# Kernel tuning notes

Hardware: AMD Instinct MI355X
Metric: run time of the kernel (lower is better)

The kernel has to match this reference:

```python
import jax, jax.numpy as jnp
import numpy as np

B, N, ESM_DIM, D, K = 256, 100000, 1280, 512, 8
ATT_TAU = 1.0
NEG_INF_FILL = -10000.0
EPS = 1e-6


def _l2norm(x, axis=-1):
    return x / jnp.linalg.norm(x, axis=axis, keepdims=True).clip(1e-12)


def setup_inputs() -> dict:
    key = jax.random.key(0)
    ks = jax.random.split(key, 8)
    index_emb = _l2norm(jax.random.normal(ks[0], (N, ESM_DIM), jnp.float32))
    return {
        "query_esm_pooled": jax.random.normal(ks[1], (B, ESM_DIM), jnp.float32),
        "model_embs": jax.random.normal(ks[2], (B, D), jnp.float32),
        "index_emb": index_emb,
        "index_labels": jax.random.randint(ks[3], (N,), 0, 2, jnp.int64),
        "exclude_idx": jax.random.randint(ks[4], (B,), 0, N, jnp.int64),
        "proj_W": jax.random.normal(ks[5], (ESM_DIM, D), jnp.float32) * 0.02,
        "proj_b": jnp.zeros((D,), jnp.float32),
        "clf_W": jax.random.normal(ks[6], (2 * D, 2), jnp.float32) * 0.02,
        "clf_b": jnp.zeros((2,), jnp.float32),
    }


def reference(query_esm_pooled, model_embs, index_emb, index_labels, exclude_idx,
              proj_W, proj_b, clf_W, clf_b):
    # esm_dim != model_emb_dim -> use ESM-pooled queries, project neighbors
    Q = _l2norm(query_esm_pooled)                       # [B, E]
    sims = Q @ index_emb.T                              # [B, N] cosine (index pre-normalized)
    sims = sims.at[jnp.arange(B), exclude_idx].set(NEG_INF_FILL)
    _, topk = jax.lax.top_k(sims, K)                    # [B, K]

    neigh_raw = index_emb[topk]                         # [B, K, E]
    neigh_lbl = index_labels[topk]                      # [B, K]
    neigh_proj = neigh_raw @ proj_W + proj_b            # [B, K, D]

    # tiny cross-attention: query = model_embs, keys/values = neighbors
    scale = 1.0 / (jnp.sqrt(jnp.float32(D)) * ATT_TAU)
    att = jax.nn.softmax(jnp.einsum('bd,bkd->bk', model_embs, neigh_proj) * scale, axis=-1)
    z_neigh = jnp.einsum('bk,bkd->bd', att, neigh_proj)  # [B, D]

    logits_retr = jnp.concatenate([model_embs, z_neigh], axis=1) @ clf_W + clf_b  # [B, 2]

    # prototypes (detached, matching torch.no_grad)
    mask_pos = (neigh_lbl == 1).astype(jnp.float32)     # [B, K]
    mask_neg = (neigh_lbl == 0).astype(jnp.float32)
    pos_proto = jnp.einsum('bk,bkd->bd', mask_pos, neigh_proj) / (mask_pos.sum(1, keepdims=True) + EPS)
    neg_proto = jnp.einsum('bk,bkd->bd', mask_neg, neigh_proj) / (mask_neg.sum(1, keepdims=True) + EPS)
    pos_proto = jax.lax.stop_gradient(pos_proto)
    neg_proto = jax.lax.stop_gradient(neg_proto)

    retr_align_loss = jnp.mean((model_embs - pos_proto) ** 2) - 0.5 * jnp.mean((model_embs - neg_proto) ** 2)
    return logits_retr, retr_align_loss
```

## Files before the change

### kernel.cpp

```cpp
#include <hip/hip_runtime.h>
#include <math.h>

#define B_SZ 256
#define N_SZ 100000
#define E_SZ 1280
#define D_SZ 512

#define NCH 1563

typedef __attribute__((ext_vector_type(8))) short s8v;
typedef __attribute__((ext_vector_type(4))) float f32x4;

__device__ __forceinline__ unsigned short f2bf(float f) {
  unsigned int u = __float_as_uint(f);
  u += 0x7fffu + ((u >> 16) & 1u);
  return (unsigned short)(u >> 16);
}
__device__ __forceinline__ unsigned int pack2(float a, float b) {
  return (unsigned)f2bf(a) | ((unsigned)f2bf(b) << 16);
}

__device__ __forceinline__ void gload16(const void* g, void* l) {
  __builtin_amdgcn_global_load_lds(
      (const __attribute__((address_space(1))) void*)g,
      (__attribute__((address_space(3))) void*)l, 16, 0, 0);
}

#define TOP8_UPDATE(v_, i_)                                                 \
  if ((v_) > minv) {                                                        \
    _Pragma("unroll")                                                       \
    for (int s_ = 0; s_ < 8; ++s_)                                          \
      if (s_ == mins) { bv[s_] = (v_); bi[s_] = (i_); }                     \
    minv = bv[0]; mins = 0;                                                 \
    _Pragma("unroll")                                                       \
    for (int s_ = 1; s_ < 8; ++s_)                                          \
      if (bv[s_] < minv) { minv = bv[s_]; mins = s_; }                      \
  }

__global__ __launch_bounds__(256) void k_normq(const float* __restrict__ q,
                                               unsigned short* __restrict__ qn) {
  __shared__ float red[4];
  int row = blockIdx.x, t = threadIdx.x;
  const float* src = q + (size_t)row * E_SZ;
  float x[5];
  float ss = 0.f;
#pragma unroll
  for (int i = 0; i < 5; ++i) { x[i] = src[t + 256 * i]; ss += x[i] * x[i]; }
#pragma unroll
  for (int o = 32; o > 0; o >>= 1) ss += __shfl_down(ss, o, 64);
  if ((t & 63) == 0) red[t >> 6] = ss;
  __syncthreads();
  float nrm = sqrtf(red[0] + red[1] + red[2] + red[3]);
  nrm = fmaxf(nrm, 1e-12f);
  float inv = 1.0f / nrm;
  unsigned short* dst = qn + (size_t)row * E_SZ;
#pragma unroll
  for (int i = 0; i < 5; ++i) dst[t + 256 * i] = f2bf(x[i] * inv);
}

__global__ __launch_bounds__(256) void k_wt(const float* __restrict__ W,
                                            unsigned short* __restrict__ Wt) {
  __shared__ float T[64][65];
  const int kb = blockIdx.x * 64;
  const int nb = blockIdx.y * 64;
  const int t = threadIdx.x;
#pragma unroll
  for (int i = 0; i < 16; ++i) {
    int kr = i * 4 + (t >> 6);
    T[kr][t & 63] = W[(size_t)(kb + kr) * D_SZ + nb + (t & 63)];
  }
  __syncthreads();
  const int n = t >> 2, ks = (t & 3) * 16;
  unsigned int ow[8];
#pragma unroll
  for (int j = 0; j < 8; ++j)
    ow[j] = (unsigned)f2bf(T[ks + 2 * j][n]) |
            ((unsigned)f2bf(T[ks + 2 * j + 1][n]) << 16);
  unsigned short* dst = Wt + (size_t)(nb + n) * E_SZ + kb + ks;
  *(uint4*)dst = make_uint4(ow[0], ow[1], ow[2], ow[3]);
  *(uint4*)(dst + 8) = make_uint4(ow[4], ow[5], ow[6], ow[7]);
}

__global__ __launch_bounds__(256) void k_sims_topk(
    const unsigned short* __restrict__ qn, const float* __restrict__ emb,
    const int* __restrict__ excl, float* __restrict__ cval) {
  __shared__ __align__(16) char lds[40960];
  const int t = threadIdx.x;
  const int l = t & 63, w = t >> 6;
  const int r15 = l & 15, g = l >> 4;
  const int jbase = blockIdx.x * 64;
  const int myq = (w << 6) + l;
  const int ex = excl[myq];

  f32x4 acc[4][4];
#pragma unroll
  for (int i = 0; i < 4; ++i)
#pragma unroll
    for (int j = 0; j < 4; ++j) acc[i][j] = (f32x4)0.f;

  const int chunk = (t & 3) ^ ((t >> 3) & 3);
  const unsigned short* aSrc0 = qn + (size_t)(t >> 2) * E_SZ + chunk * 8;
  const int grow = min(jbase + (t >> 2), N_SZ - 1);
  const float* bSrc = emb + (size_t)grow * E_SZ + chunk * 8;
  const int bwr = t * 16;

  const int fsw = ((g ^ ((r15 >> 1) & 3)) << 4);
  int afoff[4], bfoff[4];
#pragma unroll
  for (int mq = 0; mq < 4; ++mq)
    afoff[mq] = ((w << 6) + mq * 16 + r15) * 64 + fsw;
#pragma unroll
  for (int nj = 0; nj < 4; ++nj)
    bfoff[nj] = (nj * 16 + r15) * 64 + fsw;

  float4 bw0[2], bw1[2];

#define STAGEA(kt_, aoff_)                                                   \
  { _Pragma("unroll") for (int i_ = 0; i_ < 4; ++i_)                         \
      gload16(aSrc0 + (size_t)i_ * (64 * E_SZ) + (kt_),                      \
              lds + (aoff_) + i_ * 4096 + w * 1024); }
#define LOADB(br_, kt_)                                                      \
  { br_[0] = *(const float4*)(bSrc + (kt_));                                 \
    br_[1] = *(const float4*)(bSrc + (kt_) + 4); }
#define CVTWR(br_, boff_)                                                    \
  { uint4 p_;                                                                \
    p_.x = pack2(br_[0].x, br_[0].y); p_.y = pack2(br_[0].z, br_[0].w);      \
    p_.z = pack2(br_[1].x, br_[1].y); p_.w = pack2(br_[1].z, br_[1].w);      \
    *(uint4*)(lds + (boff_) + bwr) = p_; }
#define COMPUTE(aoff_, boff_)                                                \
  { s8v af_[4];                                                              \
    _Pragma("unroll") for (int mq_ = 0; mq_ < 4; ++mq_)                      \
      af_[mq_] = *(const s8v*)(lds + (aoff_) + afoff[mq_]);                  \
    _Pragma("unroll") for (int nj_ = 0; nj_ < 4; ++nj_) {                    \
      s8v bf_ = *(const s8v*)(lds + (boff_) + bfoff[nj_]);                   \
      _Pragma("unroll") for (int mq_ = 0; mq_ < 4; ++mq_)                    \
        acc[mq_][nj_] = __builtin_amdgcn_mfma_f32_16x16x32_bf16(             \
            af_[mq_], bf_, acc[mq_][nj_], 0, 0, 0);                          \
    } }
#define FENCE2                                                               \
  { asm volatile("s_waitcnt vmcnt(2) lgkmcnt(0)" ::: "memory");              \
    __builtin_amdgcn_s_barrier(); }
#define FENCE0                                                               \
  { asm volatile("s_waitcnt vmcnt(0) lgkmcnt(0)" ::: "memory");              \
    __builtin_amdgcn_s_barrier(); }

  STAGEA(0, 0);
  LOADB(bw0, 0);
  LOADB(bw1, 32);
  CVTWR(bw0, 32768);
  FENCE2;

  for (int s = 0; s < 40; s += 2) {
    STAGEA((s + 1) * 32, 16384);
    if (s + 2 < 40) LOADB(bw0, (s + 2) * 32);
    COMPUTE(0, 32768);
    CVTWR(bw1, 36864);
    if (s + 2 < 40) { FENCE2; } else { FENCE0; }
    if (s + 2 < 40) STAGEA((s + 2) * 32, 0);
    if (s + 3 < 40) LOADB(bw1, (s + 3) * 32);
    COMPUTE(16384, 36864);
    if (s + 2 < 40) CVTWR(bw0, 32768);
    if (s + 3 < 40) { FENCE2; } else { FENCE0; }
  }

  for (int ph = 0; ph < 2; ++ph) {
    if ((w >> 1) == ph) {
      float* Sbuf = (float*)(lds + (w & 1) * 16640);
#pragma unroll
      for (int mq = 0; mq < 4; ++mq)
#pragma unroll
        for (int nj = 0; nj < 4; ++nj)
#pragma unroll
          for (int r = 0; r < 4; ++r)
            Sbuf[(16 * mq + 4 * g + r) * 65 + 16 * nj + r15] = acc[mq][nj][r];
      float bv[8]; int bi[8];
#pragma unroll
      for (int s = 0; s < 8; ++s) { bv[s] = -1e30f; bi[s] = 0; }
      float minv = -1e30f; int mins = 0;
      const float* Srow = Sbuf + l * 65;
      for (int c = 0; c < 64; ++c) {
        int gj = jbase + c;
        float v = Srow[c];
        if (gj < N_SZ && gj != ex) { TOP8_UPDATE(v, gj); }
      }
      float* vdst = cval + (size_t)blockIdx.x * 4096 + myq * 8;
      *(float4*)vdst = make_float4(bv[0], bv[1], bv[2], bv[3]);
      *(float4*)(vdst + 4) = make_float4(bv[4], bv[5], bv[6], bv[7]);
      int* idst = (int*)(cval + (size_t)blockIdx.x * 4096 + 2048) + myq * 8;
      *(int4*)idst = make_int4(bi[0], bi[1], bi[2], bi[3]);
      *(int4*)(idst + 4) = make_int4(bi[4], bi[5], bi[6], bi[7]);
    }
    __syncthreads();
  }
#undef STAGEA
#undef LOADB
#undef CVTWR
#undef COMPUTE
#undef FENCE2
#undef FENCE0
}

__global__ __launch_bounds__(256) void k_merge(const float* __restrict__ cval,
                                               int* __restrict__ topk) {
  __shared__ float sv[2048];
  __shared__ int si[2048];
  const int q = blockIdx.x, t = threadIdx.x;
  float bv[8]; int bi[8];
#pragma unroll
  for (int s = 0; s < 8; ++s) { bv[s] = -1e30f; bi[s] = 0; }
  float minv = -1e30f; int mins = 0;
  for (int c = t; c < NCH; c += 256) {
    const float* vp = cval + (size_t)c * 4096 + q * 8;
    const int* ip = (const int*)(cval + (size_t)c * 4096 + 2048) + q * 8;
    float4 v0 = *(const float4*)vp, v1 = *(const float4*)(vp + 4);
    int4 i0 = *(const int4*)ip, i1 = *(const int4*)(ip + 4);
    float va[8] = {v0.x, v0.y, v0.z, v0.w, v1.x, v1.y, v1.z, v1.w};
    int ia[8] = {i0.x, i0.y, i0.z, i0.w, i1.x, i1.y, i1.z, i1.w};
#pragma unroll
    for (int s = 0; s < 8; ++s) {
      float v = va[s]; int ix = ia[s];
      TOP8_UPDATE(v, ix);
    }
  }
#pragma unroll
  for (int s = 0; s < 8; ++s) { sv[t * 8 + s] = bv[s]; si[t * 8 + s] = bi[s]; }
  __syncthreads();
  if (t < 64) {
    for (int rr = 1; rr < 4; ++rr) {
      int r = t + rr * 64;
#pragma unroll
      for (int s = 0; s < 8; ++s) {
        float v = sv[r * 8 + s]; int ix = si[r * 8 + s];
        TOP8_UPDATE(v, ix);
      }
    }
#pragma unroll
    for (int s = 0; s < 8; ++s) { sv[t * 8 + s] = bv[s]; si[t * 8 + s] = bi[s]; }
  }
  __syncthreads();
  if (t < 8) {
    for (int rr = 1; rr < 8; ++rr) {
      int r = t + rr * 8;
#pragma unroll
      for (int s = 0; s < 8; ++s) {
        float v = sv[r * 8 + s]; int ix = si[r * 8 + s];
        TOP8_UPDATE(v, ix);
      }
    }
#pragma unroll
    for (int s = 0; s < 8; ++s) { sv[t * 8 + s] = bv[s]; si[t * 8 + s] = bi[s]; }
  }
  __syncthreads();
  if (t == 0) {
    for (int r = 1; r < 8; ++r) {
#pragma unroll
      for (int s = 0; s < 8; ++s) {
        float v = sv[r * 8 + s]; int ix = si[r * 8 + s];
        TOP8_UPDATE(v, ix);
      }
    }
#pragma unroll
    for (int s = 0; s < 8; ++s) topk[q * 8 + s] = bi[s];
  }
}

__global__ __launch_bounds__(256) void k_proj(
    const float* __restrict__ emb, const int* __restrict__ topk,
    const unsigned short* __restrict__ Wt, const float* __restrict__ bias,
    float* __restrict__ nproj) {
  __shared__ __align__(16) char lds[65536];
  const int t = threadIdx.x, l = t & 63, w = t >> 6;
  const int r15 = l & 15, g = l >> 4;
  const int wm = w >> 1, wn = w & 1;
  const int r0 = blockIdx.x * 128, n0 = blockIdx.y * 128;
  const int sr = t >> 3, kc = t & 7;

  int grow[4];
#pragma unroll
  for (int i = 0; i < 4; ++i) grow[i] = topk[r0 + i * 32 + sr];

  int woff[4];
#pragma unroll
  for (int i = 0; i < 4; ++i) {
    int row = i * 32 + sr;
    woff[i] = row * 128 + (((kc + (row & 7)) & 7) << 4);
  }
  int afoff[2][4], bfoff[2][4];
#pragma unroll
  for (int h = 0; h < 2; ++h) {
#pragma unroll
    for (int qq = 0; qq < 4; ++qq) {
      int rowa = 64 * wm + 16 * qq + r15;
      afoff[h][qq] = rowa * 128 + ((((h << 2) + g + (rowa & 7)) & 7) << 4);
      int rowb = 64 * wn + 16 * qq + r15;
      bfoff[h][qq] = rowb * 128 + ((((h << 2) + g + (rowb & 7)) & 7) << 4);
    }
  }

  f32x4 acc[4][4];
#pragma unroll
  for (int i = 0; i < 4; ++i)
#pragma unroll
    for (int j = 0; j < 4; ++j) acc[i][j] = (f32x4)0.f;

  float4 aset[4][2];
  s8v bset[4];

#define PLOADA(kt_)                                                          \
  { _Pragma("unroll") for (int i_ = 0; i_ < 4; ++i_) {                       \
      const float* s_ = emb + (size_t)grow[i_] * E_SZ + (kt_) + kc * 8;      \
      aset[i_][0] = *(const float4*)s_;                                      \
      aset[i_][1] = *(const float4*)(s_ + 4); } }
#define PLOADB(kt_)                                                          \
  { _Pragma("unroll") for (int i_ = 0; i_ < 4; ++i_)                         \
      bset[i_] = *(const s8v*)(Wt + (size_t)(n0 + i_ * 32 + sr) * E_SZ +     \
                               (kt_) + kc * 8); }
#define PWR(bA_, bB_)                                                        \
  { _Pragma("unroll") for (int i_ = 0; i_ < 4; ++i_) {                       \
      uint4 p_;                                                              \
      p_.x = pack2(aset[i_][0].x, aset[i_][0].y);                            \
      p_.y = pack2(aset[i_][0].z, aset[i_][0].w);                            \
      p_.z = pack2(aset[i_][1].x, aset[i_][1].y);                            \
      p_.w = pack2(aset[i_][1].z, aset[i_][1].w);                            \
      *(uint4*)((bA_) + woff[i_]) = p_;                                      \
      *(s8v*)((bB_) + woff[i_]) = bset[i_]; } }
#define PCOMP(bA_, bB_)                                                      \
  { _Pragma("unroll") for (int h_ = 0; h_ < 2; ++h_) {                       \
      s8v af_[4], bf_[4];                                                    \
      _Pragma("unroll") for (int q_ = 0; q_ < 4; ++q_) {                     \
        af_[q_] = *(const s8v*)((bA_) + afoff[h_][q_]);                      \
        bf_[q_] = *(const s8v*)((bB_) + bfoff[h_][q_]); }                    \
      _Pragma("unroll") for (int nj_ = 0; nj_ < 4; ++nj_)                    \
        _Pragma("unroll") for (int mq_ = 0; mq_ < 4; ++mq_)                  \
          acc[mq_][nj_] = __builtin_amdgcn_mfma_f32_16x16x32_bf16(           \
              af_[mq_], bf_[nj_], acc[mq_][nj_], 0, 0, 0); } }

  PLOADA(0); PLOADB(0);
  PWR(lds, lds + 32768);
  __syncthreads();
  for (int s = 0; s < 20; ++s) {
    char* cA = lds + (s & 1) * 16384;
    char* cB = lds + 32768 + (s & 1) * 16384;
    char* nA = lds + ((s + 1) & 1) * 16384;
    char* nB = lds + 32768 + ((s + 1) & 1) * 16384;
    if (s + 1 < 20) { PLOADA((s + 1) * 64); PLOADB((s + 1) * 64); }
    PCOMP(cA, cB);
    if (s + 1 < 20) { PWR(nA, nB); }
    __syncthreads();
  }
#pragma unroll
  for (int nj = 0; nj < 4; ++nj) {
    int n = n0 + 64 * wn + 16 * nj + r15;
    float bn = bias[n];
#pragma unroll
    for (int mq = 0; mq < 4; ++mq) {
      int m = r0 + 64 * wm + 16 * mq + 4 * g;
#pragma unroll
      for (int r = 0; r < 4; ++r)
        nproj[(size_t)(m + r) * D_SZ + n] = acc[mq][nj][r] + bn;
    }
  }
#undef PLOADA
#undef PLOADB
#undef PWR
#undef PCOMP
}

__global__ __launch_bounds__(256) void k_attn(
    const float* __restrict__ model, const float* __restrict__ proj,
    const int* __restrict__ topk, const int* __restrict__ labels,
    const float* __restrict__ clfW, const float* __restrict__ clfb,
    float* __restrict__ out, float* __restrict__ lossp) {
  __shared__ float P[8 * 512];
  __shared__ float red[4];
  int b = blockIdx.x, t = threadIdx.x;
  const float* src = proj + (size_t)b * 8 * 512;
#pragma unroll
  for (int i = 0; i < 4; ++i) {
    int o = i * 1024 + t * 4;
    *(float4*)&P[o] = *(const float4*)&src[o];
  }
  __syncthreads();
  float m0 = model[b * 512 + t], m1 = model[b * 512 + 256 + t];

  float sc[8];
#pragma unroll
  for (int k = 0; k < 8; ++k) {
    float p = m0 * P[k * 512 + t] + m1 * P[k * 512 + 256 + t];
#pragma unroll
    for (int o = 32; o > 0; o >>= 1) p += __shfl_down(p, o, 64);
    if ((t & 63) == 0) red[t >> 6] = p;
    __syncthreads();
    sc[k] = red[0] + red[1] + red[2] + red[3];
    __syncthreads();
  }
  const float scale = 0.04419417382415922f;
  float mx = -1e30f;
  float s_[8];
#pragma unroll
  for (int k = 0; k < 8; ++k) { s_[k] = sc[k] * scale; mx = fmaxf(mx, s_[k]); }
  float den = 0.f, att[8];
#pragma unroll
  for (int k = 0; k < 8; ++k) { att[k] = expf(s_[k] - mx); den += att[k]; }
  float iden = 1.0f / den;
#pragma unroll
  for (int k = 0; k < 8; ++k) att[k] *= iden;

  float z0 = 0.f, z1 = 0.f;
#pragma unroll
  for (int k = 0; k < 8; ++k) {
    z0 = fmaf(att[k], P[k * 512 + t], z0);
    z1 = fmaf(att[k], P[k * 512 + 256 + t], z1);
  }
#pragma unroll
  for (int c = 0; c < 2; ++c) {
    float lp = m0 * clfW[t * 2 + c] + m1 * clfW[(t + 256) * 2 + c] +
               z0 * clfW[(512 + t) * 2 + c] + z1 * clfW[(768 + t) * 2 + c];
#pragma unroll
    for (int o = 32; o > 0; o >>= 1) lp += __shfl_down(lp, o, 64);
    if ((t & 63) == 0) red[t >> 6] = lp;
    __syncthreads();
    if (t == 0) out[b * 2 + c] = red[0] + red[1] + red[2] + red[3] + clfb[c];
    __syncthreads();
  }
  float cp = 0.f, cn = 0.f;
  float p0 = 0.f, p1 = 0.f, n0 = 0.f, n1 = 0.f;
#pragma unroll
  for (int k = 0; k < 8; ++k) {
    int lb = labels[topk[b * 8 + k]];
    float mp = (lb == 1) ? 1.f : 0.f;
    float mn = (lb == 0) ? 1.f : 0.f;
    cp += mp; cn += mn;
    p0 = fmaf(mp, P[k * 512 + t], p0);
    p1 = fmaf(mp, P[k * 512 + 256 + t], p1);
    n0 = fmaf(mn, P[k * 512 + t], n0);
    n1 = fmaf(mn, P[k * 512 + 256 + t], n1);
  }
  float icp = 1.0f / (cp + 1e-6f), icn = 1.0f / (cn + 1e-6f);
  p0 *= icp; p1 *= icp; n0 *= icn; n1 *= icn;
  float lq = (m0 - p0) * (m0 - p0) + (m1 - p1) * (m1 - p1) -
             0.5f * ((m0 - n0) * (m0 - n0) + (m1 - n1) * (m1 - n1));
#pragma unroll
  for (int o = 32; o > 0; o >>= 1) lq += __shfl_down(lq, o, 64);
  if ((t & 63) == 0) red[t >> 6] = lq;
  __syncthreads();
  if (t == 0) lossp[b] = red[0] + red[1] + red[2] + red[3];
}

__global__ __launch_bounds__(256) void k_loss(const float* __restrict__ lossp,
                                              float* __restrict__ out) {
  __shared__ float red[4];
  int t = threadIdx.x;
  float v = lossp[t];
#pragma unroll
  for (int o = 32; o > 0; o >>= 1) v += __shfl_down(v, o, 64);
  if ((t & 63) == 0) red[t >> 6] = v;
  __syncthreads();
  if (t == 0)
    out[512] = (red[0] + red[1] + red[2] + red[3]) * (1.0f / (256.0f * 512.0f));
}

extern "C" void kernel_launch(void* const* d_in, const int* in_sizes, int n_in,
                              void* d_out, int out_size, void* d_ws,
                              size_t ws_size, hipStream_t stream) {
  (void)in_sizes; (void)n_in; (void)out_size; (void)ws_size;
  const float* q      = (const float*)d_in[0];
  const float* model  = (const float*)d_in[1];
  const float* emb    = (const float*)d_in[2];
  const int*   labels = (const int*)d_in[3];
  const int*   excl   = (const int*)d_in[4];
  const float* projW  = (const float*)d_in[5];
  const float* projb  = (const float*)d_in[6];
  const float* clfW   = (const float*)d_in[7];
  const float* clfb   = (const float*)d_in[8];
  float* out = (float*)d_out;

  char* ws = (char*)d_ws;
  unsigned short* qn = (unsigned short*)ws;
  unsigned short* Wt = (unsigned short*)(ws + 655360);
  float* cval  = (float*)(ws + 1966080);
  int*   topk  = (int*)(ws + 27574272);
  float* nproj = (float*)(ws + 27582464);
  float* lossp = (float*)(ws + 31776768);

  k_normq<<<256, 256, 0, stream>>>(q, qn);
  k_wt<<<dim3(20, 8), 256, 0, stream>>>(projW, Wt);
  k_sims_topk<<<NCH, 256, 0, stream>>>(qn, emb, excl, cval);
  k_merge<<<256, 256, 0, stream>>>(cval, topk);
  k_proj<<<dim3(16, 4), 256, 0, stream>>>(emb, topk, Wt, projb, nproj);
  k_attn<<<256, 256, 0, stream>>>(model, nproj, topk, labels, clfW, clfb, out, lossp);
  k_loss<<<1, 256, 0, stream>>>(lossp, out);
}
```

Before: 412.1 us.

## Load MFMA operands directly from global into registers, bypassing LDS staging

Replaces the LDS-staged, barrier-synchronised double-buffered GEMM in the similarity/top-k kernel with direct global-to-register loads of the A and B fragments, register double-buffering and no per-step barriers. The fp32-to-bf16 packing now uses the HIP bf16 intrinsic. The epilogue scan switches to a 68-float padded row read as float4. This removes LDS traffic and barrier stalls, but every wave now fetches its own copy of the shared B tile and the query rows. That multiplies global and L2 traffic and raises register pressure.

```diff
diff --git a/kernel.cpp b/kernel.cpp
--- a/kernel.cpp
+++ b/kernel.cpp
@@ -1,4 +1,5 @@
 #include <hip/hip_runtime.h>
+#include <hip/hip_bf16.h>
 #include <math.h>
 
 #define B_SZ 256
@@ -17,13 +18,9 @@
   return (unsigned short)(u >> 16);
 }
 __device__ __forceinline__ unsigned int pack2(float a, float b) {
-  return (unsigned)f2bf(a) | ((unsigned)f2bf(b) << 16);
-}
-
-__device__ __forceinline__ void gload16(const void* g, void* l) {
-  __builtin_amdgcn_global_load_lds(
-      (const __attribute__((address_space(1))) void*)g,
-      (__attribute__((address_space(3))) void*)l, 16, 0, 0);
+  union { __hip_bfloat162 h; unsigned u; } c;
+  c.h = __float22bfloat162_rn(make_float2(a, b));
+  return c.u;
 }
 
 #define TOP8_UPDATE(v_, i_)                                                 \
@@ -84,7 +81,7 @@
 __global__ __launch_bounds__(256) void k_sims_topk(
     const unsigned short* __restrict__ qn, const float* __restrict__ emb,
     const int* __restrict__ excl, float* __restrict__ cval) {
-  __shared__ __align__(16) char lds[40960];
+  __shared__ __align__(16) float Sbuf[2][64 * 68];
   const int t = threadIdx.x;
   const int l = t & 63, w = t >> 6;
   const int r15 = l & 15, g = l >> 4;
@@ -98,90 +95,89 @@
 #pragma unroll
     for (int j = 0; j < 4; ++j) acc[i][j] = (f32x4)0.f;
 
-  const int chunk = (t & 3) ^ ((t >> 3) & 3);
-  const unsigned short* aSrc0 = qn + (size_t)(t >> 2) * E_SZ + chunk * 8;
-  const int grow = min(jbase + (t >> 2), N_SZ - 1);
-  const float* bSrc = emb + (size_t)grow * E_SZ + chunk * 8;
-  const int bwr = t * 16;
-
-  const int fsw = ((g ^ ((r15 >> 1) & 3)) << 4);
-  int afoff[4], bfoff[4];
+  const unsigned short* aP[4];
 #pragma unroll
   for (int mq = 0; mq < 4; ++mq)
-    afoff[mq] = ((w << 6) + mq * 16 + r15) * 64 + fsw;
-#pragma unroll
-  for (int nj = 0; nj < 4; ++nj)
-    bfoff[nj] = (nj * 16 + r15) * 64 + fsw;
-
-  float4 bw0[2], bw1[2];
-
-#define STAGEA(kt_, aoff_)                                                   \
+    aP[mq] = qn + (size_t)((w << 6) + 16 * mq + r15) * E_SZ + g * 8;
+  const float* bP[4];
+#pragma unroll
+  for (int nj = 0; nj < 4; ++nj) {
+    int jr = min(jbase + 16 * nj + r15, N_SZ - 1);
+    bP[nj] = emb + (size_t)jr * E_SZ + g * 8;
+  }
+
+  s8v aA[4], aB[4];
+  float4 braw[4][2];
+
+#define LOADA(dst_, kt_)                                                     \
   { _Pragma("unroll") for (int i_ = 0; i_ < 4; ++i_)                         \
-      gload16(aSrc0 + (size_t)i_ * (64 * E_SZ) + (kt_),                      \
-              lds + (aoff_) + i_ * 4096 + w * 1024); }
-#define LOADB(br_, kt_)                                                      \
-  { br_[0] = *(const float4*)(bSrc + (kt_));                                 \
-    br_[1] = *(const float4*)(bSrc + (kt_) + 4); }
-#define CVTWR(br_, boff_)                                                    \
-  { uint4 p_;                                                                \
-    p_.x = pack2(br_[0].x, br_[0].y); p_.y = pack2(br_[0].z, br_[0].w);      \
-    p_.z = pack2(br_[1].x, br_[1].y); p_.w = pack2(br_[1].z, br_[1].w);      \
-    *(uint4*)(lds + (boff_) + bwr) = p_; }
-#define COMPUTE(aoff_, boff_)                                                \
-  { s8v af_[4];                                                              \
-    _Pragma("unroll") for (int mq_ = 0; mq_ < 4; ++mq_)                      \
-      af_[mq_] = *(const s8v*)(lds + (aoff_) + afoff[mq_]);                  \
-    _Pragma("unroll") for (int nj_ = 0; nj_ < 4; ++nj_) {                    \
-      s8v bf_ = *(const s8v*)(lds + (boff_) + bfoff[nj_]);                   \
+      dst_[i_] = *(const s8v*)(aP[i_] + (kt_)); }
+#define LOADB(kt_)                                                           \
+  { _Pragma("unroll") for (int i_ = 0; i_ < 4; ++i_) {                       \
+      braw[i_][0] = *(const float4*)(bP[i_] + (kt_));                        \
+      braw[i_][1] = *(const float4*)(bP[i_] + (kt_) + 4); } }
+#define PACKB(bb_)                                                           \
+  { _Pragma("unroll") for (int i_ = 0; i_ < 4; ++i_) {                       \
+      union { uint4 u; s8v s; } c_;                                          \
+      c_.u.x = pack2(braw[i_][0].x, braw[i_][0].y);                          \
+      c_.u.y = pack2(braw[i_][0].z, braw[i_][0].w);                          \
+      c_.u.z = pack2(braw[i_][1].x, braw[i_][1].y);                          \
+      c_.u.w = pack2(braw[i_][1].z, braw[i_][1].w);                          \
+      bb_[i_] = c_.s; } }
+#define MFMA16(a_, bb_)                                                      \
+  { _Pragma("unroll") for (int nj_ = 0; nj_ < 4; ++nj_)                      \
       _Pragma("unroll") for (int mq_ = 0; mq_ < 4; ++mq_)                    \
         acc[mq_][nj_] = __builtin_amdgcn_mfma_f32_16x16x32_bf16(             \
-            af_[mq_], bf_, acc[mq_][nj_], 0, 0, 0);                          \
-    } }
-#define FENCE2                                                               \
-  { asm volatile("s_waitcnt vmcnt(2) lgkmcnt(0)" ::: "memory");              \
-    __builtin_amdgcn_s_barrier(); }
-#define FENCE0                                                               \
-  { asm volatile("s_waitcnt vmcnt(0) lgkmcnt(0)" ::: "memory");              \
-    __builtin_amdgcn_s_barrier(); }
-
-  STAGEA(0, 0);
-  LOADB(bw0, 0);
-  LOADB(bw1, 32);
-  CVTWR(bw0, 32768);
-  FENCE2;
+            a_[mq_], bb_[nj_], acc[mq_][nj_], 0, 0, 0); }
+
+  LOADA(aA, 0);
+  LOADB(0);
 
   for (int s = 0; s < 40; s += 2) {
-    STAGEA((s + 1) * 32, 16384);
-    if (s + 2 < 40) LOADB(bw0, (s + 2) * 32);
-    COMPUTE(0, 32768);
-    CVTWR(bw1, 36864);
-    if (s + 2 < 40) { FENCE2; } else { FENCE0; }
-    if (s + 2 < 40) STAGEA((s + 2) * 32, 0);
-    if (s + 3 < 40) LOADB(bw1, (s + 3) * 32);
-    COMPUTE(16384, 36864);
-    if (s + 2 < 40) CVTWR(bw0, 32768);
-    if (s + 3 < 40) { FENCE2; } else { FENCE0; }
-  }
-
+    {
+      s8v bb[4];
+      PACKB(bb);
+      LOADA(aB, (s + 1) * 32);
+      LOADB((s + 1) * 32);
+      MFMA16(aA, bb);
+    }
+    {
+      s8v bb[4];
+      PACKB(bb);
+      if (s + 2 < 40) { LOADA(aA, (s + 2) * 32); LOADB((s + 2) * 32); }
+      MFMA16(aB, bb);
+    }
+  }
+#undef LOADA
+#undef LOADB
+#undef PACKB
+#undef MFMA16
+
+  __syncthreads();
   for (int ph = 0; ph < 2; ++ph) {
     if ((w >> 1) == ph) {
-      float* Sbuf = (float*)(lds + (w & 1) * 16640);
+      float* S = &Sbuf[w & 1][0];
 #pragma unroll
       for (int mq = 0; mq < 4; ++mq)
 #pragma unroll
         for (int nj = 0; nj < 4; ++nj)
 #pragma unroll
           for (int r = 0; r < 4; ++r)
-            Sbuf[(16 * mq + 4 * g + r) * 65 + 16 * nj + r15] = acc[mq][nj][r];
+            S[(16 * mq + 4 * g + r) * 68 + 16 * nj + r15] = acc[mq][nj][r];
       float bv[8]; int bi[8];
 #pragma unroll
       for (int s = 0; s < 8; ++s) { bv[s] = -1e30f; bi[s] = 0; }
       float minv = -1e30f; int mins = 0;
-      const float* Srow = Sbuf + l * 65;
-      for (int c = 0; c < 64; ++c) {
-        int gj = jbase + c;
-        float v = Srow[c];
-        if (gj < N_SZ && gj != ex) { TOP8_UPDATE(v, gj); }
+      const float* Srow = S + l * 68;
+      for (int c4 = 0; c4 < 16; ++c4) {
+        float4 v4 = *(const float4*)(Srow + c4 * 4);
+        float va[4] = {v4.x, v4.y, v4.z, v4.w};
+#pragma unroll
+        for (int u = 0; u < 4; ++u) {
+          int gj = jbase + c4 * 4 + u;
+          float v = va[u];
+          if (gj < N_SZ && gj != ex) { TOP8_UPDATE(v, gj); }
+        }
       }
       float* vdst = cval + (size_t)blockIdx.x * 4096 + myq * 8;
       *(float4*)vdst = make_float4(bv[0], bv[1], bv[2], bv[3]);
@@ -192,12 +188,6 @@
     }
     __syncthreads();
   }
-#undef STAGEA
-#undef LOADB
-#undef CVTWR
-#undef COMPUTE
-#undef FENCE2
-#undef FENCE0
 }
 
 __global__ __launch_bounds__(256) void k_merge(const float* __restrict__ cval,
```

New measurement: 538.7 us. +30.7%, slower.

## Widen similarity tile to 128 index rows with 512-thread blocks and in-block candidate merge

Applied to the files above, without the earlier changes.

The similarity+top-k kernel now processes 128 index rows per block with 8 waves (512 threads), so each block reuses the staged query tile across twice as many index rows and halves the block count. Per-block partial top-8 lists are merged in LDS before being written in a per-query layout, which halves the candidate volume the merge kernel reads and makes its reads contiguous. It also fuses the query-normalisation and weight-transpose kernels into one launch, swaps in a hardware bf16 pack intrinsic, and reorders the pipeline with sched barriers and a padded B layout. The cost is more LDS per block, a serialized multi-phase epilogue, and 512-thread blocks.

```diff
diff --git a/kernel.cpp b/kernel.cpp
--- a/kernel.cpp
+++ b/kernel.cpp
@@ -1,4 +1,5 @@
 #include <hip/hip_runtime.h>
+#include <hip/hip_bf16.h>
 #include <math.h>
 
 #define B_SZ 256
@@ -6,7 +7,7 @@
 #define E_SZ 1280
 #define D_SZ 512
 
-#define NCH 1563
+#define NCH2 782
 
 typedef __attribute__((ext_vector_type(8))) short s8v;
 typedef __attribute__((ext_vector_type(4))) float f32x4;
@@ -17,9 +18,10 @@
   return (unsigned short)(u >> 16);
 }
 __device__ __forceinline__ unsigned int pack2(float a, float b) {
-  return (unsigned)f2bf(a) | ((unsigned)f2bf(b) << 16);
-}
-
+  union { __hip_bfloat162 h; unsigned u; } c;
+  c.h = __float22bfloat162_rn(make_float2(a, b));
+  return c.u;
+}
 __device__ __forceinline__ void gload16(const void* g, void* l) {
   __builtin_amdgcn_global_load_lds(
       (const __attribute__((address_space(1))) void*)g,
@@ -37,60 +39,62 @@
       if (bv[s_] < minv) { minv = bv[s_]; mins = s_; }                      \
   }
 
-__global__ __launch_bounds__(256) void k_normq(const float* __restrict__ q,
-                                               unsigned short* __restrict__ qn) {
-  __shared__ float red[4];
-  int row = blockIdx.x, t = threadIdx.x;
-  const float* src = q + (size_t)row * E_SZ;
-  float x[5];
-  float ss = 0.f;
-#pragma unroll
-  for (int i = 0; i < 5; ++i) { x[i] = src[t + 256 * i]; ss += x[i] * x[i]; }
-#pragma unroll
-  for (int o = 32; o > 0; o >>= 1) ss += __shfl_down(ss, o, 64);
-  if ((t & 63) == 0) red[t >> 6] = ss;
-  __syncthreads();
-  float nrm = sqrtf(red[0] + red[1] + red[2] + red[3]);
-  nrm = fmaxf(nrm, 1e-12f);
-  float inv = 1.0f / nrm;
-  unsigned short* dst = qn + (size_t)row * E_SZ;
-#pragma unroll
-  for (int i = 0; i < 5; ++i) dst[t + 256 * i] = f2bf(x[i] * inv);
-}
-
-__global__ __launch_bounds__(256) void k_wt(const float* __restrict__ W,
-                                            unsigned short* __restrict__ Wt) {
-  __shared__ float T[64][65];
-  const int kb = blockIdx.x * 64;
-  const int nb = blockIdx.y * 64;
+__global__ __launch_bounds__(256) void k_prep(const float* __restrict__ q,
+                                              unsigned short* __restrict__ qn,
+                                              const float* __restrict__ W,
+                                              unsigned short* __restrict__ Wt) {
+  __shared__ __align__(16) char sm[64 * 65 * 4];
   const int t = threadIdx.x;
-#pragma unroll
-  for (int i = 0; i < 16; ++i) {
-    int kr = i * 4 + (t >> 6);
-    T[kr][t & 63] = W[(size_t)(kb + kr) * D_SZ + nb + (t & 63)];
-  }
-  __syncthreads();
-  const int n = t >> 2, ks = (t & 3) * 16;
-  unsigned int ow[8];
-#pragma unroll
-  for (int j = 0; j < 8; ++j)
-    ow[j] = (unsigned)f2bf(T[ks + 2 * j][n]) |
-            ((unsigned)f2bf(T[ks + 2 * j + 1][n]) << 16);
-  unsigned short* dst = Wt + (size_t)(nb + n) * E_SZ + kb + ks;
-  *(uint4*)dst = make_uint4(ow[0], ow[1], ow[2], ow[3]);
-  *(uint4*)(dst + 8) = make_uint4(ow[4], ow[5], ow[6], ow[7]);
-}
-
-__global__ __launch_bounds__(256) void k_sims_topk(
+  if (blockIdx.x < 256) {
+    float* red = (float*)sm;
+    int row = blockIdx.x;
+    const float* src = q + (size_t)row * E_SZ;
+    float x[5];
+    float ss = 0.f;
+#pragma unroll
+    for (int i = 0; i < 5; ++i) { x[i] = src[t + 256 * i]; ss += x[i] * x[i]; }
+#pragma unroll
+    for (int o = 32; o > 0; o >>= 1) ss += __shfl_down(ss, o, 64);
+    if ((t & 63) == 0) red[t >> 6] = ss;
+    __syncthreads();
+    float nrm = sqrtf(red[0] + red[1] + red[2] + red[3]);
+    nrm = fmaxf(nrm, 1e-12f);
+    float inv = 1.0f / nrm;
+    unsigned short* dst = qn + (size_t)row * E_SZ;
+#pragma unroll
+    for (int i = 0; i < 5; ++i) dst[t + 256 * i] = f2bf(x[i] * inv);
+  } else {
+    float (*T)[65] = (float(*)[65])sm;
+    int idx = blockIdx.x - 256;
+    int kb = (idx % 20) * 64;
+    int nb = (idx / 20) * 64;
+#pragma unroll
+    for (int i = 0; i < 16; ++i) {
+      int kr = i * 4 + (t >> 6);
+      T[kr][t & 63] = W[(size_t)(kb + kr) * D_SZ + nb + (t & 63)];
+    }
+    __syncthreads();
+    const int n = t >> 2, ks = (t & 3) * 16;
+    unsigned int ow[8];
+#pragma unroll
+    for (int j = 0; j < 8; ++j)
+      ow[j] = (unsigned)f2bf(T[ks + 2 * j][n]) |
+              ((unsigned)f2bf(T[ks + 2 * j + 1][n]) << 16);
+    unsigned short* dst = Wt + (size_t)(nb + n) * E_SZ + kb + ks;
+    *(uint4*)dst = make_uint4(ow[0], ow[1], ow[2], ow[3]);
+    *(uint4*)(dst + 8) = make_uint4(ow[4], ow[5], ow[6], ow[7]);
+  }
+}
+
+__global__ __launch_bounds__(512, 2) void k_sims_topk(
     const unsigned short* __restrict__ qn, const float* __restrict__ emb,
-    const int* __restrict__ excl, float* __restrict__ cval) {
-  __shared__ __align__(16) char lds[40960];
+    const int* __restrict__ excl, float* __restrict__ cvalv,
+    int* __restrict__ cvali) {
+  __shared__ __align__(16) char lds[53248];
   const int t = threadIdx.x;
   const int l = t & 63, w = t >> 6;
   const int r15 = l & 15, g = l >> 4;
-  const int jbase = blockIdx.x * 64;
-  const int myq = (w << 6) + l;
-  const int ex = excl[myq];
+  const int jbase = blockIdx.x * 128;
 
   f32x4 acc[4][4];
 #pragma unroll
@@ -98,35 +102,47 @@
 #pragma unroll
     for (int j = 0; j < 4; ++j) acc[i][j] = (f32x4)0.f;
 
-  const int chunk = (t & 3) ^ ((t >> 3) & 3);
-  const unsigned short* aSrc0 = qn + (size_t)(t >> 2) * E_SZ + chunk * 8;
-  const int grow = min(jbase + (t >> 2), N_SZ - 1);
-  const float* bSrc = emb + (size_t)grow * E_SZ + chunk * 8;
-  const int bwr = t * 16;
-
-  const int fsw = ((g ^ ((r15 >> 1) & 3)) << 4);
-  int afoff[4], bfoff[4];
+  const int fsw = ((g ^ (r15 & 3) ^ ((r15 >> 2) & 3)) << 4);
+  int afoff[4];
 #pragma unroll
   for (int mq = 0; mq < 4; ++mq)
-    afoff[mq] = ((w << 6) + mq * 16 + r15) * 64 + fsw;
+    afoff[mq] = (64 * (w >> 1) + 16 * mq + r15) * 64 + fsw;
+  int bfoff[4];
 #pragma unroll
   for (int nj = 0; nj < 4; ++nj)
-    bfoff[nj] = (nj * 16 + r15) * 64 + fsw;
-
-  float4 bw0[2], bw1[2];
-
-#define STAGEA(kt_, aoff_)                                                   \
-  { _Pragma("unroll") for (int i_ = 0; i_ < 4; ++i_)                         \
-      gload16(aSrc0 + (size_t)i_ * (64 * E_SZ) + (kt_),                      \
-              lds + (aoff_) + i_ * 4096 + w * 1024); }
-#define LOADB(br_, kt_)                                                      \
-  { br_[0] = *(const float4*)(bSrc + (kt_));                                 \
-    br_[1] = *(const float4*)(bSrc + (kt_) + 4); }
-#define CVTWR(br_, boff_)                                                    \
+    bfoff[nj] = (64 * (w & 1) + 16 * nj + r15) * 80 + (g << 4);
+
+  size_t aoffs0, aoffs1;
+  int adst0, adst1;
+  {
+    int p0 = t, p1 = 512 + t;
+    int row0 = p0 >> 2, row1 = p1 >> 2;
+    int sw0 = (row0 & 3) ^ ((row0 >> 2) & 3);
+    int sw1 = (row1 & 3) ^ ((row1 >> 2) & 3);
+    aoffs0 = (size_t)row0 * E_SZ + (((p0 & 3) ^ sw0) * 8);
+    aoffs1 = (size_t)row1 * E_SZ + (((p1 & 3) ^ sw1) * 8);
+    adst0 = p0 * 16;
+    adst1 = p1 * 16;
+  }
+
+  const int brow = t >> 2, bchunk = t & 3;
+  const int bgrow = min(jbase + brow, N_SZ - 1);
+  const float* bSrc = emb + (size_t)bgrow * E_SZ + bchunk * 8;
+  const int bwoff = brow * 80 + bchunk * 16;
+
+  float4 bs0[2], bs1[2];
+
+#define STAGEA(kt_, dstoff_)                                                 \
+  { gload16(qn + aoffs0 + (kt_), lds + (dstoff_) + adst0);                   \
+    gload16(qn + aoffs1 + (kt_), lds + (dstoff_) + adst1); }
+#define LOADB(set_, kt_)                                                     \
+  { set_[0] = *(const float4*)(bSrc + (kt_));                                \
+    set_[1] = *(const float4*)(bSrc + (kt_) + 4); }
+#define CVTWR(set_, boff_)                                                   \
   { uint4 p_;                                                                \
-    p_.x = pack2(br_[0].x, br_[0].y); p_.y = pack2(br_[0].z, br_[0].w);      \
-    p_.z = pack2(br_[1].x, br_[1].y); p_.w = pack2(br_[1].z, br_[1].w);      \
-    *(uint4*)(lds + (boff_) + bwr) = p_; }
+    p_.x = pack2(set_[0].x, set_[0].y); p_.y = pack2(set_[0].z, set_[0].w);  \
+    p_.z = pack2(set_[1].x, set_[1].y); p_.w = pack2(set_[1].z, set_[1].w);  \
+    *(uint4*)(lds + (boff_) + bwoff) = p_; }
 #define COMPUTE(aoff_, boff_)                                                \
   { s8v af_[4];                                                              \
     _Pragma("unroll") for (int mq_ = 0; mq_ < 4; ++mq_)                      \
@@ -137,70 +153,103 @@
         acc[mq_][nj_] = __builtin_amdgcn_mfma_f32_16x16x32_bf16(             \
             af_[mq_], bf_, acc[mq_][nj_], 0, 0, 0);                          \
     } }
-#define FENCE2                                                               \
-  { asm volatile("s_waitcnt vmcnt(2) lgkmcnt(0)" ::: "memory");              \
-    __builtin_amdgcn_s_barrier(); }
-#define FENCE0                                                               \
-  { asm volatile("s_waitcnt vmcnt(0) lgkmcnt(0)" ::: "memory");              \
-    __builtin_amdgcn_s_barrier(); }
 
   STAGEA(0, 0);
-  LOADB(bw0, 0);
-  LOADB(bw1, 32);
-  CVTWR(bw0, 32768);
-  FENCE2;
+  __builtin_amdgcn_sched_barrier(0);
+  LOADB(bs0, 0);
+  LOADB(bs1, 32);
+  CVTWR(bs0, 32768);
+  asm volatile("s_waitcnt vmcnt(2) lgkmcnt(0)" ::: "memory");
+  __builtin_amdgcn_s_barrier();
 
   for (int s = 0; s < 40; s += 2) {
     STAGEA((s + 1) * 32, 16384);
-    if (s + 2 < 40) LOADB(bw0, (s + 2) * 32);
+    __builtin_amdgcn_sched_barrier(0);
+    if (s + 2 < 40) LOADB(bs0, (s + 2) * 32);
+    CVTWR(bs1, 43008);
     COMPUTE(0, 32768);
-    CVTWR(bw1, 36864);
-    if (s + 2 < 40) { FENCE2; } else { FENCE0; }
-    if (s + 2 < 40) STAGEA((s + 2) * 32, 0);
-    if (s + 3 < 40) LOADB(bw1, (s + 3) * 32);
-    COMPUTE(16384, 36864);
-    if (s + 2 < 40) CVTWR(bw0, 32768);
-    if (s + 3 < 40) { FENCE2; } else { FENCE0; }
-  }
-
-  for (int ph = 0; ph < 2; ++ph) {
-    if ((w >> 1) == ph) {
-      float* Sbuf = (float*)(lds + (w & 1) * 16640);
-#pragma unroll
-      for (int mq = 0; mq < 4; ++mq)
-#pragma unroll
-        for (int nj = 0; nj < 4; ++nj)
-#pragma unroll
-          for (int r = 0; r < 4; ++r)
-            Sbuf[(16 * mq + 4 * g + r) * 65 + 16 * nj + r15] = acc[mq][nj][r];
-      float bv[8]; int bi[8];
-#pragma unroll
-      for (int s = 0; s < 8; ++s) { bv[s] = -1e30f; bi[s] = 0; }
-      float minv = -1e30f; int mins = 0;
-      const float* Srow = Sbuf + l * 65;
-      for (int c = 0; c < 64; ++c) {
-        int gj = jbase + c;
-        float v = Srow[c];
-        if (gj < N_SZ && gj != ex) { TOP8_UPDATE(v, gj); }
-      }
-      float* vdst = cval + (size_t)blockIdx.x * 4096 + myq * 8;
-      *(float4*)vdst = make_float4(bv[0], bv[1], bv[2], bv[3]);
-      *(float4*)(vdst + 4) = make_float4(bv[4], bv[5], bv[6], bv[7]);
-      int* idst = (int*)(cval + (size_t)blockIdx.x * 4096 + 2048) + myq * 8;
-      *(int4*)idst = make_int4(bi[0], bi[1], bi[2], bi[3]);
-      *(int4*)(idst + 4) = make_int4(bi[4], bi[5], bi[6], bi[7]);
-    }
-    __syncthreads();
+    if (s + 2 < 40) {
+      asm volatile("s_waitcnt vmcnt(2) lgkmcnt(0)" ::: "memory");
+    } else {
+      asm volatile("s_waitcnt vmcnt(0) lgkmcnt(0)" ::: "memory");
+    }
+    __builtin_amdgcn_s_barrier();
+    if (s + 2 < 40) {
+      STAGEA((s + 2) * 32, 0);
+      __builtin_amdgcn_sched_barrier(0);
+    }
+    if (s + 3 < 40) LOADB(bs1, (s + 3) * 32);
+    if (s + 2 < 40) CVTWR(bs0, 32768);
+    COMPUTE(16384, 43008);
+    if (s + 3 < 40) {
+      asm volatile("s_waitcnt vmcnt(2) lgkmcnt(0)" ::: "memory");
+    } else if (s + 2 < 40) {
+      asm volatile("s_waitcnt vmcnt(0) lgkmcnt(0)" ::: "memory");
+    } else {
+      asm volatile("s_waitcnt lgkmcnt(0)" ::: "memory");
+    }
+    __builtin_amdgcn_s_barrier();
   }
 #undef STAGEA
 #undef LOADB
 #undef CVTWR
 #undef COMPUTE
-#undef FENCE2
-#undef FENCE0
-}
-
-__global__ __launch_bounds__(256) void k_merge(const float* __restrict__ cval,
+
+  float* S = (float*)lds;
+  float* cV = (float*)(lds + 40960);
+  int*   cI = (int*)(lds + 45056);
+  for (int ph = 0; ph < 4; ++ph) {
+    if ((w >> 1) == ph) {
+      int jcol = 64 * (w & 1);
+#pragma unroll
+      for (int mq = 0; mq < 4; ++mq)
+#pragma unroll
+        for (int nj = 0; nj < 4; ++nj)
+#pragma unroll
+          for (int r = 0; r < 4; ++r)
+            S[(16 * mq + 4 * g + r) * 132 + jcol + 16 * nj + r15] =
+                acc[mq][nj][r];
+    }
+    __syncthreads();
+    if (t < 128) {
+      int qrow = t >> 1, half = t & 1;
+      int q = ph * 64 + qrow;
+      int ex = excl[q];
+      float bv[8]; int bi[8];
+#pragma unroll
+      for (int s = 0; s < 8; ++s) { bv[s] = -1e30f; bi[s] = 0; }
+      float minv = -1e30f; int mins = 0;
+      const float* Srow = S + qrow * 132 + half * 64;
+      int j0 = jbase + half * 64;
+      for (int c = 0; c < 64; ++c) {
+        int gj = j0 + c;
+        float v = Srow[c];
+        if (gj < N_SZ && gj != ex) { TOP8_UPDATE(v, gj); }
+      }
+#pragma unroll
+      for (int s = 0; s < 8; ++s) { cV[t * 8 + s] = bv[s]; cI[t * 8 + s] = bi[s]; }
+    }
+    __syncthreads();
+    if (t < 64) {
+      int q = ph * 64 + t;
+      float bv[8]; int bi[8];
+#pragma unroll
+      for (int s = 0; s < 8; ++s) { bv[s] = -1e30f; bi[s] = 0; }
+      float minv = -1e30f; int mins = 0;
+      for (int n = 0; n < 16; ++n) {
+        float v = cV[t * 16 + n]; int ix = cI[t * 16 + n];
+        TOP8_UPDATE(v, ix);
+      }
+      size_t base = ((size_t)q * NCH2 + blockIdx.x) * 8;
+#pragma unroll
+      for (int s = 0; s < 8; ++s) { cvalv[base + s] = bv[s]; cvali[base + s] = bi[s]; }
+    }
+    __syncthreads();
+  }
+}
+
+__global__ __launch_bounds__(256) void k_merge(const float* __restrict__ cvalv,
+                                               const int* __restrict__ cvali,
                                                int* __restrict__ topk) {
   __shared__ float sv[2048];
   __shared__ int si[2048];
@@ -209,9 +258,9 @@
 #pragma unroll
   for (int s = 0; s < 8; ++s) { bv[s] = -1e30f; bi[s] = 0; }
   float minv = -1e30f; int mins = 0;
-  for (int c = t; c < NCH; c += 256) {
-    const float* vp = cval + (size_t)c * 4096 + q * 8;
-    const int* ip = (const int*)(cval + (size_t)c * 4096 + 2048) + q * 8;
+  for (int c = t; c < NCH2; c += 256) {
+    const float* vp = cvalv + ((size_t)q * NCH2 + c) * 8;
+    const int* ip = cvali + ((size_t)q * NCH2 + c) * 8;
     float4 v0 = *(const float4*)vp, v1 = *(const float4*)(vp + 4);
     int4 i0 = *(const int4*)ip, i1 = *(const int4*)(ip + 4);
     float va[8] = {v0.x, v0.y, v0.z, v0.w, v1.x, v1.y, v1.z, v1.w};
@@ -478,15 +527,15 @@
   char* ws = (char*)d_ws;
   unsigned short* qn = (unsigned short*)ws;
   unsigned short* Wt = (unsigned short*)(ws + 655360);
-  float* cval  = (float*)(ws + 1966080);
-  int*   topk  = (int*)(ws + 27574272);
-  float* nproj = (float*)(ws + 27582464);
-  float* lossp = (float*)(ws + 31776768);
-
-  k_normq<<<256, 256, 0, stream>>>(q, qn);
-  k_wt<<<dim3(20, 8), 256, 0, stream>>>(projW, Wt);
-  k_sims_topk<<<NCH, 256, 0, stream>>>(qn, emb, excl, cval);
-  k_merge<<<256, 256, 0, stream>>>(cval, topk);
+  float* cvalv = (float*)(ws + 1966080);
+  int*   cvali = (int*)(ws + 8372224);
+  int*   topk  = (int*)(ws + 14778368);
+  float* nproj = (float*)(ws + 14786560);
+  float* lossp = (float*)(ws + 18980864);
+
+  k_prep<<<416, 256, 0, stream>>>(q, qn, projW, Wt);
+  k_sims_topk<<<NCH2, 512, 0, stream>>>(qn, emb, excl, cvalv, cvali);
+  k_merge<<<256, 256, 0, stream>>>(cvalv, cvali, topk);
   k_proj<<<dim3(16, 4), 256, 0, stream>>>(emb, topk, Wt, projb, nproj);
   k_attn<<<256, 256, 0, stream>>>(model, nproj, topk, labels, clfW, clfb, out, lossp);
   k_loss<<<1, 256, 0, stream>>>(lossp, out);
```

New measurement: 571.0 us. +38.6%, slower.
